# Kernel optimization log

Measured on AMD Instinct MI355X. Metric: run time of the kernel, lower is better.

Reference implementation:

```python
import jax, jax.numpy as jnp
import numpy as np

N_NODES = 100000
N_EDGES = 1600000
N_GRAPHS = 1024
D = 128
L = 3
BN_EPS = 1e-5


def setup_inputs() -> dict:
    key = jax.random.key(0)
    ks = jax.random.split(key, 16)
    x = jax.random.normal(ks[0], (N_NODES, D), dtype=jnp.float32)
    edge_index = jax.random.randint(ks[1], (2, N_EDGES), 0, N_NODES, dtype=jnp.int64)
    batch = jnp.sort(jax.random.randint(ks[2], (N_NODES,), 0, N_GRAPHS, dtype=jnp.int64))
    w = lambda k, shape: jax.random.normal(k, shape, dtype=jnp.float32) * 0.05
    return {
        "x": x,
        "edge_index": edge_index,
        "batch": batch,
        "conv_W1": w(ks[3], (L, D, D)),
        "conv_b1": w(ks[4], (L, D)),
        "bn_gamma": jax.random.uniform(ks[5], (L, D), dtype=jnp.float32) + 0.5,
        "bn_beta": w(ks[6], (L, D)),
        "bn_mean": w(ks[7], (L, D)),
        "bn_var": jax.random.uniform(ks[8], (L, D), dtype=jnp.float32) + 0.5,
        "conv_W2": w(ks[9], (L, D, D)),
        "conv_b2": w(ks[10], (L, D)),
        "head_W1": w(ks[11], (D, D)),
        "head_b1": w(ks[12], (D,)),
        "head_W2": w(ks[13], (D, D)),
        "head_b2": w(ks[14], (D,)),
    }


def reference(x, edge_index, batch, conv_W1, conv_b1, bn_gamma, bn_beta,
              bn_mean, bn_var, conv_W2, conv_b2, head_W1, head_b1,
              head_W2, head_b2):
    n = x.shape[0]
    src, dst = edge_index[0], edge_index[1]
    for l in range(L):
        # GINConv, eps=0: nn(x + sum_{j->i} x_j)
        agg = jax.ops.segment_sum(x[src], dst, num_segments=n)  # [N, D]
        h = x + agg
        # MLP([in, h, h]): Linear -> BatchNorm(eval) -> ReLU -> Linear
        h = h @ conv_W1[l] + conv_b1[l]
        h = (h - bn_mean[l]) * jax.lax.rsqrt(bn_var[l] + BN_EPS) * bn_gamma[l] + bn_beta[l]
        h = jax.nn.relu(h)
        h = h @ conv_W2[l] + conv_b2[l]
        x = jax.nn.relu(h)  # .relu() in the outer forward
    # global_add_pool over graph ids
    g = jax.ops.segment_sum(x, batch, num_segments=N_GRAPHS)  # [B, D]
    # head MLP (norm=None, dropout inactive at eval): Linear -> ReLU -> Linear
    g = jax.nn.relu(g @ head_W1 + head_b1)
    return g @ head_W2 + head_b2
```

## Files before the change

### kernel.cpp

```cpp
#include <hip/hip_runtime.h>

#define N_NODES  100000
#define N_EDGES  1600000
#define N_GRAPHS 1024
#define D        128
#define BN_EPS   1e-5f

#define FNSLICE      98
#define FSLICE_NODES 1024
#define FSLICE_CAP   20480
#define QCAP         96
#define CCHUNK       4000
#define CGRID        400

#define CVT_BLOCKS   6250
#define PW_BLOCKS    384
#define FOLD_BLOCKS  3
#define GST_BLOCKS   5
#define SETUP_GRID   (CVT_BLOCKS + PW_BLOCKS + FOLD_BLOCKS + GST_BLOCKS + 1)

typedef short bf16x8 __attribute__((ext_vector_type(8)));
typedef float f32x4  __attribute__((ext_vector_type(4)));

__device__ __forceinline__ ushort f2bf(float f) {
    unsigned int b = __float_as_uint(f);
    return (ushort)((b + 0x7fffu + ((b >> 16) & 1u)) >> 16);
}
__device__ __forceinline__ float bflo(unsigned int u) { return __uint_as_float(u << 16); }
__device__ __forceinline__ float bfhi(unsigned int u) { return __uint_as_float(u & 0xffff0000u); }
__device__ __forceinline__ unsigned int packbf(float x, float y) {
    return (unsigned int)f2bf(x) | ((unsigned int)f2bf(y) << 16);
}

__global__ __launch_bounds__(256) void setup_kernel(
        const float* __restrict__ x, ushort* __restrict__ xb,
        const float* __restrict__ W1, const float* __restrict__ W2,
        ushort* __restrict__ Wt,
        const float* __restrict__ b1, const float* __restrict__ gamma,
        const float* __restrict__ beta, const float* __restrict__ mean,
        const float* __restrict__ var, const float* __restrict__ b2,
        float* __restrict__ folds,
        const int* __restrict__ batch, int* __restrict__ gstart,
        int* __restrict__ slice_tail, int* __restrict__ offsets) {
    int b = blockIdx.x, t = threadIdx.x;
    if (b < CVT_BLOCKS) {
        size_t i = ((size_t)b * 256 + t) * 8;
        float4 v0 = *(const float4*)(x + i);
        float4 v1 = *(const float4*)(x + i + 4);
        uint4 o;
        o.x = packbf(v0.x, v0.y); o.y = packbf(v0.z, v0.w);
        o.z = packbf(v1.x, v1.y); o.w = packbf(v1.z, v1.w);
        *(uint4*)(xb + i) = o;
    } else if (b < CVT_BLOCKS + PW_BLOCKS) {
        int idx = (b - CVT_BLOCKS) * 256 + t;
        int i = idx >> 14, r = idx & 16383;
        int n = r >> 7, k = r & 127, l = i >> 1;
        const float* W = (i & 1) ? (W2 + (size_t)l * D * D) : (W1 + (size_t)l * D * D);
        Wt[idx] = f2bf(W[k * D + n]);
    } else if (b < CVT_BLOCKS + PW_BLOCKS + FOLD_BLOCKS) {
        int idx = (b - CVT_BLOCKS - PW_BLOCKS) * 256 + t;
        if (idx < 6 * D) {
            int i = idx >> 7, j = idx & 127, l = i >> 1;
            float s, o;
            if ((i & 1) == 0) {
                float sv = gamma[l * D + j] * rsqrtf(var[l * D + j] + BN_EPS);
                s = sv;
                o = (b1[l * D + j] - mean[l * D + j]) * sv + beta[l * D + j];
            } else {
                s = 1.0f;
                o = b2[l * D + j];
            }
            folds[(size_t)i * 2 * D + j]     = s;
            folds[(size_t)i * 2 * D + D + j] = o;
        }
    } else if (b < CVT_BLOCKS + PW_BLOCKS + FOLD_BLOCKS + GST_BLOCKS) {
        int g = (b - CVT_BLOCKS - PW_BLOCKS - FOLD_BLOCKS) * 256 + t;
        if (g <= N_GRAPHS) {
            int lo = 0, hi = N_NODES;
            while (lo < hi) {
                int mid = (lo + hi) >> 1;
                if (batch[mid] < g) lo = mid + 1; else hi = mid;
            }
            gstart[g] = lo;
        }
    } else {
        if (t < FNSLICE) slice_tail[t] = 0;
        if (t == 255) offsets[N_NODES] = N_EDGES;
    }
}

__global__ __launch_bounds__(256) void compact_kernel(const int* __restrict__ src,
                                                      const int* __restrict__ dst,
                                                      unsigned int* __restrict__ squeue,
                                                      int* __restrict__ slice_tail) {
    __shared__ unsigned int qbuf[FNSLICE * QCAP];
    __shared__ int qcnt[FNSLICE];
    __shared__ int qbase[FNSLICE];
    int t = threadIdx.x;
    for (int i = t; i < FNSLICE; i += 256) qcnt[i] = 0;
    __syncthreads();
    int e0 = blockIdx.x * CCHUNK;
    int eend = e0 + CCHUNK; if (eend > N_EDGES) eend = N_EDGES;
    for (int e = e0 + t; e < eend; e += 256) {
        int d = dst[e], s = src[e];
        int sl = d >> 10;
        unsigned int pk = ((unsigned int)(d & 1023) << 17) | (unsigned int)s;
        int pos = atomicAdd(&qcnt[sl], 1);
        if (pos < QCAP) qbuf[sl * QCAP + pos] = pk;
        else {
            int gp = atomicAdd(&slice_tail[sl], 1);
            squeue[(size_t)sl * FSLICE_CAP + gp] = pk;
        }
    }
    __syncthreads();
    for (int i = t; i < FNSLICE; i += 256) {
        int n = qcnt[i]; if (n > QCAP) n = QCAP;
        qbase[i] = atomicAdd(&slice_tail[i], n);
    }
    __syncthreads();
    int wv = t >> 6, ln = t & 63;
    for (int sl = wv; sl < FNSLICE; sl += 4) {
        int n = qcnt[sl]; if (n > QCAP) n = QCAP;
        int gb = qbase[sl];
        for (int i = ln; i < n; i += 64)
            squeue[(size_t)sl * FSLICE_CAP + gb + i] = qbuf[sl * QCAP + i];
    }
}

__global__ __launch_bounds__(1024) void fill_local(const unsigned int* __restrict__ squeue,
                                                   const int* __restrict__ slice_tail,
                                                   int* __restrict__ offsets,
                                                   int* __restrict__ csr_src) {
    __shared__ int hist[FSLICE_NODES];
    __shared__ int cur[FSLICE_NODES];
    __shared__ int sbase[128];
    __shared__ int wsum[16];
    int sl = blockIdx.x, t = threadIdx.x;
    int n = slice_tail[sl];
    if (t < 128) sbase[t] = (t < FNSLICE) ? slice_tail[t] : 0;
    hist[t] = 0;
    __syncthreads();
    for (int off = 1; off < 128; off <<= 1) {
        int u = (t < 128 && t >= off) ? sbase[t - off] : 0;
        __syncthreads();
        if (t < 128) sbase[t] += u;
        __syncthreads();
    }
    int gbase = (sl == 0) ? 0 : sbase[sl - 1];
    size_t qb = (size_t)sl * FSLICE_CAP;
    for (int i = t; i < n; i += 1024)
        atomicAdd(&hist[squeue[qb + i] >> 17], 1);
    __syncthreads();
    int c = hist[t];
    int lane = t & 63, w = t >> 6;
    int sc = c;
#pragma unroll
    for (int off = 1; off < 64; off <<= 1) {
        int u = __shfl_up(sc, off, 64);
        if (lane >= off) sc += u;
    }
    if (lane == 63) wsum[w] = sc;
    __syncthreads();
    if (t < 16) {
        int ws = wsum[t];
        int s2 = ws;
#pragma unroll
        for (int off = 1; off < 16; off <<= 1) {
            int u = __shfl_up(s2, off, 16);
            if (t >= off) s2 += u;
        }
        wsum[t] = s2 - ws;
    }
    __syncthreads();
    int gslot = gbase + sc + wsum[w] - c;
    cur[t] = gslot;
    int node = sl * FSLICE_NODES + t;
    if (node < N_NODES) offsets[node] = gslot;
    __syncthreads();
    for (int i = t; i < n; i += 1024) {
        unsigned int p = squeue[qb + i];
        int slot = atomicAdd(&cur[p >> 17], 1);
        csr_src[slot] = (int)(p & 0x1FFFFu);
    }
}

__global__ __launch_bounds__(256) void gather_bf16(const ushort* __restrict__ xb,
                                                   const int* __restrict__ offsets,
                                                   const int* __restrict__ csr_src,
                                                   ushort* __restrict__ hb) {
    int wv = threadIdx.x >> 6, lane = threadIdx.x & 63;
    int node = blockIdx.x * 4 + wv;
    const unsigned int* base = (const unsigned int*)xb;
    unsigned int u = base[(size_t)node * 64 + lane];
    float ax = bflo(u), ay = bfhi(u);
    int b = offsets[node], e = offsets[node + 1];
    int i = b;
    for (; i + 15 < e; i += 16) {
        int s0 = csr_src[i],      s1 = csr_src[i + 1],  s2 = csr_src[i + 2],  s3 = csr_src[i + 3];
        int s4 = csr_src[i + 4],  s5 = csr_src[i + 5],  s6 = csr_src[i + 6],  s7 = csr_src[i + 7];
        int s8 = csr_src[i + 8],  s9 = csr_src[i + 9],  sa = csr_src[i + 10], sb = csr_src[i + 11];
        int sc = csr_src[i + 12], sd = csr_src[i + 13], se = csr_src[i + 14], sf = csr_src[i + 15];
        unsigned int v0 = base[(size_t)s0 * 64 + lane];
        unsigned int v1 = base[(size_t)s1 * 64 + lane];
        unsigned int v2 = base[(size_t)s2 * 64 + lane];
        unsigned int v3 = base[(size_t)s3 * 64 + lane];
        unsigned int v4 = base[(size_t)s4 * 64 + lane];
        unsigned int v5 = base[(size_t)s5 * 64 + lane];
        unsigned int v6 = base[(size_t)s6 * 64 + lane];
        unsigned int v7 = base[(size_t)s7 * 64 + lane];
        unsigned int v8 = base[(size_t)s8 * 64 + lane];
        unsigned int v9 = base[(size_t)s9 * 64 + lane];
        unsigned int va = base[(size_t)sa * 64 + lane];
        unsigned int vb = base[(size_t)sb * 64 + lane];
        unsigned int vc = base[(size_t)sc * 64 + lane];
        unsigned int vd = base[(size_t)sd * 64 + lane];
        unsigned int ve = base[(size_t)se * 64 + lane];
        unsigned int vf = base[(size_t)sf * 64 + lane];
        ax += bflo(v0) + bflo(v1) + bflo(v2) + bflo(v3)
            + bflo(v4) + bflo(v5) + bflo(v6) + bflo(v7)
            + bflo(v8) + bflo(v9) + bflo(va) + bflo(vb)
            + bflo(vc) + bflo(vd) + bflo(ve) + bflo(vf);
        ay += bfhi(v0) + bfhi(v1) + bfhi(v2) + bfhi(v3)
            + bfhi(v4) + bfhi(v5) + bfhi(v6) + bfhi(v7)
            + bfhi(v8) + bfhi(v9) + bfhi(va) + bfhi(vb)
            + bfhi(vc) + bfhi(vd) + bfhi(ve) + bfhi(vf);
    }
    for (; i + 3 < e; i += 4) {
        int s0 = csr_src[i], s1 = csr_src[i + 1], s2 = csr_src[i + 2], s3 = csr_src[i + 3];
        unsigned int v0 = base[(size_t)s0 * 64 + lane];
        unsigned int v1 = base[(size_t)s1 * 64 + lane];
        unsigned int v2 = base[(size_t)s2 * 64 + lane];
        unsigned int v3 = base[(size_t)s3 * 64 + lane];
        ax += bflo(v0) + bflo(v1) + bflo(v2) + bflo(v3);
        ay += bfhi(v0) + bfhi(v1) + bfhi(v2) + bfhi(v3);
    }
    for (; i < e; ++i) {
        unsigned int v = base[(size_t)csr_src[i] * 64 + lane];
        ax += bflo(v); ay += bfhi(v);
    }
    ((unsigned int*)hb)[(size_t)node * 64 + lane] = packbf(ax, ay);
}

__global__ __launch_bounds__(512, 4) void fused_gemm(const ushort* __restrict__ in,
                                                     ushort* __restrict__ out,
                                                     const ushort* __restrict__ Wt1,
                                                     const ushort* __restrict__ Wt2,
                                                     const float* __restrict__ fold1,
                                                     const float* __restrict__ fold2) {
    __shared__ ushort As[128 * 136];
    __shared__ ushort Bs[128 * 136];
    int t = threadIdx.x;
    int row0 = blockIdx.x * 128;

#pragma unroll
    for (int i = 0; i < 4; ++i) {
        int f = t + 512 * i; int m = f >> 4, g = f & 15;
        *(float4*)(As + m * 136 + g * 8) = *(const float4*)(in + (size_t)(row0 + m) * D + g * 8);
        *(float4*)(Bs + m * 136 + g * 8) = *(const float4*)(Wt1 + (size_t)m * D + g * 8);
    }
    const uint4* w2v = (const uint4*)Wt2;
    uint4 p0 = w2v[t];
    uint4 p1 = w2v[t + 512];
    uint4 p2 = w2v[t + 1024];
    uint4 p3 = w2v[t + 1536];
    __syncthreads();

    int lane = t & 63, wv = t >> 6;
    int quad = lane >> 4, mr = lane & 15;
    int mbase = wv * 16;
    const ushort* ap = As + (mbase + mr) * 136 + quad * 8;
    bf16x8 a0 = *(const bf16x8*)(ap);
    bf16x8 a1 = *(const bf16x8*)(ap + 32);
    bf16x8 a2 = *(const bf16x8*)(ap + 64);
    bf16x8 a3 = *(const bf16x8*)(ap + 96);

#pragma unroll
    for (int nt = 0; nt < 8; ++nt) {
        const ushort* bq = Bs + (nt * 16 + mr) * 136 + quad * 8;
        bf16x8 b0 = *(const bf16x8*)(bq);
        bf16x8 b1 = *(const bf16x8*)(bq + 32);
        bf16x8 b2 = *(const bf16x8*)(bq + 64);
        bf16x8 b3 = *(const bf16x8*)(bq + 96);
        f32x4 acc = {0.f, 0.f, 0.f, 0.f};
        acc = __builtin_amdgcn_mfma_f32_16x16x32_bf16(a0, b0, acc, 0, 0, 0);
        acc = __builtin_amdgcn_mfma_f32_16x16x32_bf16(a1, b1, acc, 0, 0, 0);
        acc = __builtin_amdgcn_mfma_f32_16x16x32_bf16(a2, b2, acc, 0, 0, 0);
        acc = __builtin_amdgcn_mfma_f32_16x16x32_bf16(a3, b3, acc, 0, 0, 0);
        int j = nt * 16 + mr;
        float s = fold1[j], o = fold1[D + j];
#pragma unroll
        for (int r = 0; r < 4; ++r) {
            float z = fmaxf(fmaf(acc[r], s, o), 0.0f);
            As[(mbase + quad * 4 + r) * 136 + j] = f2bf(z);
        }
    }
    __syncthreads();

    {
        int f0 = t;          *(uint4*)(Bs + (f0 >> 4) * 136 + (f0 & 15) * 8) = p0;
        int f1 = t + 512;    *(uint4*)(Bs + (f1 >> 4) * 136 + (f1 & 15) * 8) = p1;
        int f2 = t + 1024;   *(uint4*)(Bs + (f2 >> 4) * 136 + (f2 & 15) * 8) = p2;
        int f3 = t + 1536;   *(uint4*)(Bs + (f3 >> 4) * 136 + (f3 & 15) * 8) = p3;
    }
    const ushort* hp = As + (mbase + mr) * 136 + quad * 8;
    bf16x8 h0 = *(const bf16x8*)(hp);
    bf16x8 h1 = *(const bf16x8*)(hp + 32);
    bf16x8 h2 = *(const bf16x8*)(hp + 64);
    bf16x8 h3 = *(const bf16x8*)(hp + 96);
    __syncthreads();

#pragma unroll
    for (int nt = 0; nt < 8; ++nt) {
        const ushort* bq = Bs + (nt * 16 + mr) * 136 + quad * 8;
        bf16x8 b0 = *(const bf16x8*)(bq);
        bf16x8 b1 = *(const bf16x8*)(bq + 32);
        bf16x8 b2 = *(const bf16x8*)(bq + 64);
        bf16x8 b3 = *(const bf16x8*)(bq + 96);
        f32x4 acc = {0.f, 0.f, 0.f, 0.f};
        acc = __builtin_amdgcn_mfma_f32_16x16x32_bf16(h0, b0, acc, 0, 0, 0);
        acc = __builtin_amdgcn_mfma_f32_16x16x32_bf16(h1, b1, acc, 0, 0, 0);
        acc = __builtin_amdgcn_mfma_f32_16x16x32_bf16(h2, b2, acc, 0, 0, 0);
        acc = __builtin_amdgcn_mfma_f32_16x16x32_bf16(h3, b3, acc, 0, 0, 0);
        int j = nt * 16 + mr;
        float o = fold2[D + j];
#pragma unroll
        for (int r = 0; r < 4; ++r) {
            float z = fmaxf(acc[r] + o, 0.0f);
            As[(mbase + quad * 4 + r) * 136 + j] = f2bf(z);
        }
    }
    __syncthreads();

#pragma unroll
    for (int i = 0; i < 8; ++i) {
        int f = t + 512 * i; int lr = f >> 5, g = f & 31;
        if (row0 + lr < N_NODES)
            *(float2*)(out + (size_t)(row0 + lr) * D + g * 4) =
                *(const float2*)(As + lr * 136 + g * 4);
    }
}

__global__ __launch_bounds__(128) void poolhead_kernel(const ushort* __restrict__ xb,
                                                       const int* __restrict__ gstart,
                                                       const float* __restrict__ W1,
                                                       const float* __restrict__ b1,
                                                       const float* __restrict__ W2,
                                                       const float* __restrict__ b2,
                                                       float* __restrict__ out) {
    __shared__ float row[128];
    __shared__ float t1[128];
    int r = blockIdx.x, j = threadIdx.x;
    float acc = 0.0f;
    int b = gstart[r], e = gstart[r + 1];
    for (int i = b; i < e; ++i)
        acc += __uint_as_float(((unsigned int)xb[(size_t)i * D + j]) << 16);
    row[j] = acc;
    __syncthreads();
    float a1 = b1[j];
    for (int k = 0; k < D; ++k) a1 = fmaf(row[k], W1[k * D + j], a1);
    t1[j] = fmaxf(a1, 0.0f);
    __syncthreads();
    float a2 = b2[j];
    for (int k = 0; k < D; ++k) a2 = fmaf(t1[k], W2[k * D + j], a2);
    out[r * D + j] = a2;
}

extern "C" void kernel_launch(void* const* d_in, const int* in_sizes, int n_in,
                              void* d_out, int out_size, void* d_ws, size_t ws_size,
                              hipStream_t stream) {
    const float* x        = (const float*)d_in[0];
    const int*   ei       = (const int*)d_in[1];
    const int*   src      = ei;
    const int*   dst      = ei + N_EDGES;
    const int*   batch    = (const int*)d_in[2];
    const float* conv_W1  = (const float*)d_in[3];
    const float* conv_b1  = (const float*)d_in[4];
    const float* bn_gamma = (const float*)d_in[5];
    const float* bn_beta  = (const float*)d_in[6];
    const float* bn_mean  = (const float*)d_in[7];
    const float* bn_var   = (const float*)d_in[8];
    const float* conv_W2  = (const float*)d_in[9];
    const float* conv_b2  = (const float*)d_in[10];
    const float* head_W1  = (const float*)d_in[11];
    const float* head_b1  = (const float*)d_in[12];
    const float* head_W2  = (const float*)d_in[13];
    const float* head_b2  = (const float*)d_in[14];
    float* out = (float*)d_out;

    char* ws = (char*)d_ws;
    size_t off = 0;
    auto alloc = [&](size_t bytes) -> void* {
        void* p = ws + off;
        off = (off + bytes + 255) & ~(size_t)255;
        return p;
    };
    const size_t NODE_BUF = (size_t)(N_NODES + 128) * D * sizeof(ushort);
    ushort* buf0    = (ushort*)alloc(NODE_BUF);
    ushort* buf1    = (ushort*)alloc(NODE_BUF);
    ushort* Wt      = (ushort*)alloc((size_t)6 * D * D * sizeof(ushort));
    float*  folds   = (float*)alloc((size_t)6 * 2 * D * sizeof(float));
    unsigned int* squeue = (unsigned int*)alloc((size_t)FNSLICE * FSLICE_CAP * sizeof(unsigned int));
    int*   csr_src  = (int*)alloc((size_t)(N_EDGES + 64) * sizeof(int));
    int*   offsets  = (int*)alloc((size_t)(N_NODES + 1) * sizeof(int));
    int*   slice_tail = (int*)alloc((size_t)FNSLICE * sizeof(int));
    int*   gstart   = (int*)alloc((size_t)(N_GRAPHS + 1) * sizeof(int));

    setup_kernel<<<SETUP_GRID, 256, 0, stream>>>(
        x, buf0, conv_W1, conv_W2, Wt,
        conv_b1, bn_gamma, bn_beta, bn_mean, bn_var, conv_b2, folds,
        batch, gstart, slice_tail, offsets);
    compact_kernel<<<CGRID, 256, 0, stream>>>(src, dst, squeue, slice_tail);
    fill_local<<<FNSLICE, 1024, 0, stream>>>(squeue, slice_tail, offsets, csr_src);

    const int FUSED_GRID = (N_NODES + 127) / 128;
    for (int l = 0; l < 3; ++l) {
        gather_bf16<<<N_NODES / 4, 256, 0, stream>>>(buf0, offsets, csr_src, buf1);
        fused_gemm<<<FUSED_GRID, 512, 0, stream>>>(buf1, buf0,
            Wt + (size_t)(2 * l) * D * D, Wt + (size_t)(2 * l + 1) * D * D,
            folds + (size_t)(2 * l) * 2 * D, folds + (size_t)(2 * l + 1) * 2 * D);
    }

    poolhead_kernel<<<N_GRAPHS, 128, 0, stream>>>(buf0, gstart, head_W1, head_b1,
                                                  head_W2, head_b2, out);
}
```

Baseline: 445.5 us.

## Fuse neighbor gather into GEMM kernel, writing aggregates directly to LDS

Merges the separate gather kernel into the fused MLP kernel. Each wave aggregates its 16 rows of neighbor features straight into the shared-memory A tile, so the intermediate aggregate buffer is never written to or read back from global memory and one launch per layer disappears. Output buffers now ping-pong. The trade-off is that each block's MFMA stage waits on irregular gathers, and with 512-thread blocks and heavy LDS use there may be less latency hiding than the former 25000 small gather blocks had.

```diff
diff --git a/kernel.cpp b/kernel.cpp
--- a/kernel.cpp
+++ b/kernel.cpp
@@ -184,80 +184,85 @@
     }
 }
 
-__global__ __launch_bounds__(256) void gather_bf16(const ushort* __restrict__ xb,
-                                                   const int* __restrict__ offsets,
-                                                   const int* __restrict__ csr_src,
-                                                   ushort* __restrict__ hb) {
-    int wv = threadIdx.x >> 6, lane = threadIdx.x & 63;
-    int node = blockIdx.x * 4 + wv;
-    const unsigned int* base = (const unsigned int*)xb;
-    unsigned int u = base[(size_t)node * 64 + lane];
-    float ax = bflo(u), ay = bfhi(u);
-    int b = offsets[node], e = offsets[node + 1];
-    int i = b;
-    for (; i + 15 < e; i += 16) {
-        int s0 = csr_src[i],      s1 = csr_src[i + 1],  s2 = csr_src[i + 2],  s3 = csr_src[i + 3];
-        int s4 = csr_src[i + 4],  s5 = csr_src[i + 5],  s6 = csr_src[i + 6],  s7 = csr_src[i + 7];
-        int s8 = csr_src[i + 8],  s9 = csr_src[i + 9],  sa = csr_src[i + 10], sb = csr_src[i + 11];
-        int sc = csr_src[i + 12], sd = csr_src[i + 13], se = csr_src[i + 14], sf = csr_src[i + 15];
-        unsigned int v0 = base[(size_t)s0 * 64 + lane];
-        unsigned int v1 = base[(size_t)s1 * 64 + lane];
-        unsigned int v2 = base[(size_t)s2 * 64 + lane];
-        unsigned int v3 = base[(size_t)s3 * 64 + lane];
-        unsigned int v4 = base[(size_t)s4 * 64 + lane];
-        unsigned int v5 = base[(size_t)s5 * 64 + lane];
-        unsigned int v6 = base[(size_t)s6 * 64 + lane];
-        unsigned int v7 = base[(size_t)s7 * 64 + lane];
-        unsigned int v8 = base[(size_t)s8 * 64 + lane];
-        unsigned int v9 = base[(size_t)s9 * 64 + lane];
-        unsigned int va = base[(size_t)sa * 64 + lane];
-        unsigned int vb = base[(size_t)sb * 64 + lane];
-        unsigned int vc = base[(size_t)sc * 64 + lane];
-        unsigned int vd = base[(size_t)sd * 64 + lane];
-        unsigned int ve = base[(size_t)se * 64 + lane];
-        unsigned int vf = base[(size_t)sf * 64 + lane];
-        ax += bflo(v0) + bflo(v1) + bflo(v2) + bflo(v3)
-            + bflo(v4) + bflo(v5) + bflo(v6) + bflo(v7)
-            + bflo(v8) + bflo(v9) + bflo(va) + bflo(vb)
-            + bflo(vc) + bflo(vd) + bflo(ve) + bflo(vf);
-        ay += bfhi(v0) + bfhi(v1) + bfhi(v2) + bfhi(v3)
-            + bfhi(v4) + bfhi(v5) + bfhi(v6) + bfhi(v7)
-            + bfhi(v8) + bfhi(v9) + bfhi(va) + bfhi(vb)
-            + bfhi(vc) + bfhi(vd) + bfhi(ve) + bfhi(vf);
-    }
-    for (; i + 3 < e; i += 4) {
-        int s0 = csr_src[i], s1 = csr_src[i + 1], s2 = csr_src[i + 2], s3 = csr_src[i + 3];
-        unsigned int v0 = base[(size_t)s0 * 64 + lane];
-        unsigned int v1 = base[(size_t)s1 * 64 + lane];
-        unsigned int v2 = base[(size_t)s2 * 64 + lane];
-        unsigned int v3 = base[(size_t)s3 * 64 + lane];
-        ax += bflo(v0) + bflo(v1) + bflo(v2) + bflo(v3);
-        ay += bfhi(v0) + bfhi(v1) + bfhi(v2) + bfhi(v3);
-    }
-    for (; i < e; ++i) {
-        unsigned int v = base[(size_t)csr_src[i] * 64 + lane];
-        ax += bflo(v); ay += bfhi(v);
-    }
-    ((unsigned int*)hb)[(size_t)node * 64 + lane] = packbf(ax, ay);
-}
-
-__global__ __launch_bounds__(512, 4) void fused_gemm(const ushort* __restrict__ in,
-                                                     ushort* __restrict__ out,
-                                                     const ushort* __restrict__ Wt1,
-                                                     const ushort* __restrict__ Wt2,
-                                                     const float* __restrict__ fold1,
-                                                     const float* __restrict__ fold2) {
+__global__ __launch_bounds__(512, 4) void gin_layer(const ushort* __restrict__ in,
+                                                    ushort* __restrict__ out,
+                                                    const int* __restrict__ offsets,
+                                                    const int* __restrict__ csr_src,
+                                                    const ushort* __restrict__ Wt1,
+                                                    const ushort* __restrict__ Wt2,
+                                                    const float* __restrict__ fold1,
+                                                    const float* __restrict__ fold2) {
     __shared__ ushort As[128 * 136];
     __shared__ ushort Bs[128 * 136];
     int t = threadIdx.x;
     int row0 = blockIdx.x * 128;
+    int lane = t & 63, wv = t >> 6;
+    int mbase = wv * 16;
 
 #pragma unroll
     for (int i = 0; i < 4; ++i) {
         int f = t + 512 * i; int m = f >> 4, g = f & 15;
-        *(float4*)(As + m * 136 + g * 8) = *(const float4*)(in + (size_t)(row0 + m) * D + g * 8);
         *(float4*)(Bs + m * 136 + g * 8) = *(const float4*)(Wt1 + (size_t)m * D + g * 8);
     }
+
+    const unsigned int* base = (const unsigned int*)in;
+    unsigned int* asu = (unsigned int*)As;
+#pragma unroll 1
+    for (int rr = 0; rr < 16; ++rr) {
+        int node = row0 + mbase + rr;
+        float ax = 0.0f, ay = 0.0f;
+        if (node < N_NODES) {
+            unsigned int u = base[(size_t)node * 64 + lane];
+            ax = bflo(u); ay = bfhi(u);
+            int bo = offsets[node], e = offsets[node + 1];
+            int i = bo;
+            for (; i + 15 < e; i += 16) {
+                int s0 = csr_src[i],      s1 = csr_src[i + 1],  s2 = csr_src[i + 2],  s3 = csr_src[i + 3];
+                int s4 = csr_src[i + 4],  s5 = csr_src[i + 5],  s6 = csr_src[i + 6],  s7 = csr_src[i + 7];
+                int s8 = csr_src[i + 8],  s9 = csr_src[i + 9],  sa = csr_src[i + 10], sb = csr_src[i + 11];
+                int sc = csr_src[i + 12], sd = csr_src[i + 13], se = csr_src[i + 14], sf = csr_src[i + 15];
+                unsigned int v0 = base[(size_t)s0 * 64 + lane];
+                unsigned int v1 = base[(size_t)s1 * 64 + lane];
+                unsigned int v2 = base[(size_t)s2 * 64 + lane];
+                unsigned int v3 = base[(size_t)s3 * 64 + lane];
+                unsigned int v4 = base[(size_t)s4 * 64 + lane];
+                unsigned int v5 = base[(size_t)s5 * 64 + lane];
+                unsigned int v6 = base[(size_t)s6 * 64 + lane];
+                unsigned int v7 = base[(size_t)s7 * 64 + lane];
+                unsigned int v8 = base[(size_t)s8 * 64 + lane];
+                unsigned int v9 = base[(size_t)s9 * 64 + lane];
+                unsigned int va = base[(size_t)sa * 64 + lane];
+                unsigned int vb = base[(size_t)sb * 64 + lane];
+                unsigned int vc = base[(size_t)sc * 64 + lane];
+                unsigned int vd = base[(size_t)sd * 64 + lane];
+                unsigned int ve = base[(size_t)se * 64 + lane];
+                unsigned int vf = base[(size_t)sf * 64 + lane];
+                ax += bflo(v0) + bflo(v1) + bflo(v2) + bflo(v3)
+                    + bflo(v4) + bflo(v5) + bflo(v6) + bflo(v7)
+                    + bflo(v8) + bflo(v9) + bflo(va) + bflo(vb)
+                    + bflo(vc) + bflo(vd) + bflo(ve) + bflo(vf);
+                ay += bfhi(v0) + bfhi(v1) + bfhi(v2) + bfhi(v3)
+                    + bfhi(v4) + bfhi(v5) + bfhi(v6) + bfhi(v7)
+                    + bfhi(v8) + bfhi(v9) + bfhi(va) + bfhi(vb)
+                    + bfhi(vc) + bfhi(vd) + bfhi(ve) + bfhi(vf);
+            }
+            for (; i + 3 < e; i += 4) {
+                int s0 = csr_src[i], s1 = csr_src[i + 1], s2 = csr_src[i + 2], s3 = csr_src[i + 3];
+                unsigned int v0 = base[(size_t)s0 * 64 + lane];
+                unsigned int v1 = base[(size_t)s1 * 64 + lane];
+                unsigned int v2 = base[(size_t)s2 * 64 + lane];
+                unsigned int v3 = base[(size_t)s3 * 64 + lane];
+                ax += bflo(v0) + bflo(v1) + bflo(v2) + bflo(v3);
+                ay += bfhi(v0) + bfhi(v1) + bfhi(v2) + bfhi(v3);
+            }
+            for (; i < e; ++i) {
+                unsigned int v = base[(size_t)csr_src[i] * 64 + lane];
+                ax += bflo(v); ay += bfhi(v);
+            }
+        }
+        asu[(mbase + rr) * 68 + lane] = packbf(ax, ay);
+    }
+
     const uint4* w2v = (const uint4*)Wt2;
     uint4 p0 = w2v[t];
     uint4 p1 = w2v[t + 512];
@@ -265,9 +270,7 @@
     uint4 p3 = w2v[t + 1536];
     __syncthreads();
 
-    int lane = t & 63, wv = t >> 6;
     int quad = lane >> 4, mr = lane & 15;
-    int mbase = wv * 16;
     const ushort* ap = As + (mbase + mr) * 136 + quad * 8;
     bf16x8 a0 = *(const bf16x8*)(ap);
     bf16x8 a1 = *(const bf16x8*)(ap + 32);
@@ -413,13 +416,15 @@
     fill_local<<<FNSLICE, 1024, 0, stream>>>(squeue, slice_tail, offsets, csr_src);
 
     const int FUSED_GRID = (N_NODES + 127) / 128;
+    ushort* cur = buf0;
+    ushort* nxt = buf1;
     for (int l = 0; l < 3; ++l) {
-        gather_bf16<<<N_NODES / 4, 256, 0, stream>>>(buf0, offsets, csr_src, buf1);
-        fused_gemm<<<FUSED_GRID, 512, 0, stream>>>(buf1, buf0,
+        gin_layer<<<FUSED_GRID, 512, 0, stream>>>(cur, nxt, offsets, csr_src,
             Wt + (size_t)(2 * l) * D * D, Wt + (size_t)(2 * l + 1) * D * D,
             folds + (size_t)(2 * l) * 2 * D, folds + (size_t)(2 * l + 1) * 2 * D);
-    }
-
-    poolhead_kernel<<<N_GRAPHS, 128, 0, stream>>>(buf0, gstart, head_W1, head_b1,
+        ushort* tmp = cur; cur = nxt; nxt = tmp;
+    }
+
+    poolhead_kernel<<<N_GRAPHS, 128, 0, stream>>>(cur, gstart, head_W1, head_b1,
                                                   head_W2, head_b2, out);
 }
```

Measured after the change: 541.5 us. +21.5%, slower.

## Fold edge compaction into setup kernel and gather two nodes per wavefront

Applied to the files above, without the earlier changes.

The edge-compaction kernel now runs as extra blocks inside the setup launch, and slice_tail is zeroed by a memset issued beforehand. This removes one kernel launch and lets compaction overlap with conversion work. The gather kernel now has each wavefront handle two consecutive nodes, interleaving their neighbour loads 8 at a time so more independent memory requests are in flight. The cost is a smaller grid with more registers per thread, and every setup block now reserves compaction shared memory, which may reduce occupancy for the conversion blocks.

```diff
diff --git a/kernel.cpp b/kernel.cpp
--- a/kernel.cpp
+++ b/kernel.cpp
@@ -17,7 +17,11 @@
 #define PW_BLOCKS    384
 #define FOLD_BLOCKS  3
 #define GST_BLOCKS   5
-#define SETUP_GRID   (CVT_BLOCKS + PW_BLOCKS + FOLD_BLOCKS + GST_BLOCKS + 1)
+#define MISC_BASE    (CVT_BLOCKS + PW_BLOCKS + FOLD_BLOCKS + GST_BLOCKS)
+#define COMPACT_BASE (MISC_BASE + 1)
+#define SETUP_GRID   (COMPACT_BASE + CGRID)
+
+#define GATHER_GRID  12500
 
 typedef short bf16x8 __attribute__((ext_vector_type(8)));
 typedef float f32x4  __attribute__((ext_vector_type(4)));
@@ -41,7 +45,12 @@
         const float* __restrict__ var, const float* __restrict__ b2,
         float* __restrict__ folds,
         const int* __restrict__ batch, int* __restrict__ gstart,
-        int* __restrict__ slice_tail, int* __restrict__ offsets) {
+        int* __restrict__ slice_tail, int* __restrict__ offsets,
+        const int* __restrict__ src, const int* __restrict__ dst,
+        unsigned int* __restrict__ squeue) {
+    __shared__ unsigned int qbuf[FNSLICE * QCAP];
+    __shared__ int qcnt[FNSLICE];
+    __shared__ int qbase[FNSLICE];
     int b = blockIdx.x, t = threadIdx.x;
     if (b < CVT_BLOCKS) {
         size_t i = ((size_t)b * 256 + t) * 8;
@@ -73,7 +82,7 @@
             folds[(size_t)i * 2 * D + j]     = s;
             folds[(size_t)i * 2 * D + D + j] = o;
         }
-    } else if (b < CVT_BLOCKS + PW_BLOCKS + FOLD_BLOCKS + GST_BLOCKS) {
+    } else if (b < MISC_BASE) {
         int g = (b - CVT_BLOCKS - PW_BLOCKS - FOLD_BLOCKS) * 256 + t;
         if (g <= N_GRAPHS) {
             int lo = 0, hi = N_NODES;
@@ -83,47 +92,37 @@
             }
             gstart[g] = lo;
         }
+    } else if (b == MISC_BASE) {
+        if (t == 255) offsets[N_NODES] = N_EDGES;
     } else {
-        if (t < FNSLICE) slice_tail[t] = 0;
-        if (t == 255) offsets[N_NODES] = N_EDGES;
-    }
-}
-
-__global__ __launch_bounds__(256) void compact_kernel(const int* __restrict__ src,
-                                                      const int* __restrict__ dst,
-                                                      unsigned int* __restrict__ squeue,
-                                                      int* __restrict__ slice_tail) {
-    __shared__ unsigned int qbuf[FNSLICE * QCAP];
-    __shared__ int qcnt[FNSLICE];
-    __shared__ int qbase[FNSLICE];
-    int t = threadIdx.x;
-    for (int i = t; i < FNSLICE; i += 256) qcnt[i] = 0;
-    __syncthreads();
-    int e0 = blockIdx.x * CCHUNK;
-    int eend = e0 + CCHUNK; if (eend > N_EDGES) eend = N_EDGES;
-    for (int e = e0 + t; e < eend; e += 256) {
-        int d = dst[e], s = src[e];
-        int sl = d >> 10;
-        unsigned int pk = ((unsigned int)(d & 1023) << 17) | (unsigned int)s;
-        int pos = atomicAdd(&qcnt[sl], 1);
-        if (pos < QCAP) qbuf[sl * QCAP + pos] = pk;
-        else {
-            int gp = atomicAdd(&slice_tail[sl], 1);
-            squeue[(size_t)sl * FSLICE_CAP + gp] = pk;
-        }
-    }
-    __syncthreads();
-    for (int i = t; i < FNSLICE; i += 256) {
-        int n = qcnt[i]; if (n > QCAP) n = QCAP;
-        qbase[i] = atomicAdd(&slice_tail[i], n);
-    }
-    __syncthreads();
-    int wv = t >> 6, ln = t & 63;
-    for (int sl = wv; sl < FNSLICE; sl += 4) {
-        int n = qcnt[sl]; if (n > QCAP) n = QCAP;
-        int gb = qbase[sl];
-        for (int i = ln; i < n; i += 64)
-            squeue[(size_t)sl * FSLICE_CAP + gb + i] = qbuf[sl * QCAP + i];
+        for (int i = t; i < FNSLICE; i += 256) qcnt[i] = 0;
+        __syncthreads();
+        int e0 = (b - COMPACT_BASE) * CCHUNK;
+        int eend = e0 + CCHUNK; if (eend > N_EDGES) eend = N_EDGES;
+        for (int e = e0 + t; e < eend; e += 256) {
+            int d = dst[e], s = src[e];
+            int sl = d >> 10;
+            unsigned int pk = ((unsigned int)(d & 1023) << 17) | (unsigned int)s;
+            int pos = atomicAdd(&qcnt[sl], 1);
+            if (pos < QCAP) qbuf[sl * QCAP + pos] = pk;
+            else {
+                int gp = atomicAdd(&slice_tail[sl], 1);
+                squeue[(size_t)sl * FSLICE_CAP + gp] = pk;
+            }
+        }
+        __syncthreads();
+        for (int i = t; i < FNSLICE; i += 256) {
+            int n = qcnt[i]; if (n > QCAP) n = QCAP;
+            qbase[i] = atomicAdd(&slice_tail[i], n);
+        }
+        __syncthreads();
+        int wv = t >> 6, ln = t & 63;
+        for (int sl = wv; sl < FNSLICE; sl += 4) {
+            int n = qcnt[sl]; if (n > QCAP) n = QCAP;
+            int gb = qbase[sl];
+            for (int i = ln; i < n; i += 64)
+                squeue[(size_t)sl * FSLICE_CAP + gb + i] = qbuf[sl * QCAP + i];
+        }
     }
 }
 
@@ -184,22 +183,15 @@
     }
 }
 
-__global__ __launch_bounds__(256) void gather_bf16(const ushort* __restrict__ xb,
-                                                   const int* __restrict__ offsets,
-                                                   const int* __restrict__ csr_src,
-                                                   ushort* __restrict__ hb) {
-    int wv = threadIdx.x >> 6, lane = threadIdx.x & 63;
-    int node = blockIdx.x * 4 + wv;
-    const unsigned int* base = (const unsigned int*)xb;
-    unsigned int u = base[(size_t)node * 64 + lane];
-    float ax = bflo(u), ay = bfhi(u);
-    int b = offsets[node], e = offsets[node + 1];
-    int i = b;
+__device__ __forceinline__ void drain_stream(const unsigned int* __restrict__ base,
+                                             const int* __restrict__ csr,
+                                             int i, int e, int lane,
+                                             float& ax, float& ay) {
     for (; i + 15 < e; i += 16) {
-        int s0 = csr_src[i],      s1 = csr_src[i + 1],  s2 = csr_src[i + 2],  s3 = csr_src[i + 3];
-        int s4 = csr_src[i + 4],  s5 = csr_src[i + 5],  s6 = csr_src[i + 6],  s7 = csr_src[i + 7];
-        int s8 = csr_src[i + 8],  s9 = csr_src[i + 9],  sa = csr_src[i + 10], sb = csr_src[i + 11];
-        int sc = csr_src[i + 12], sd = csr_src[i + 13], se = csr_src[i + 14], sf = csr_src[i + 15];
+        int s0 = csr[i],      s1 = csr[i + 1],  s2 = csr[i + 2],  s3 = csr[i + 3];
+        int s4 = csr[i + 4],  s5 = csr[i + 5],  s6 = csr[i + 6],  s7 = csr[i + 7];
+        int s8 = csr[i + 8],  s9 = csr[i + 9],  sa = csr[i + 10], sb = csr[i + 11];
+        int sc = csr[i + 12], sd = csr[i + 13], se = csr[i + 14], sf = csr[i + 15];
         unsigned int v0 = base[(size_t)s0 * 64 + lane];
         unsigned int v1 = base[(size_t)s1 * 64 + lane];
         unsigned int v2 = base[(size_t)s2 * 64 + lane];
@@ -226,7 +218,7 @@
             + bfhi(vc) + bfhi(vd) + bfhi(ve) + bfhi(vf);
     }
     for (; i + 3 < e; i += 4) {
-        int s0 = csr_src[i], s1 = csr_src[i + 1], s2 = csr_src[i + 2], s3 = csr_src[i + 3];
+        int s0 = csr[i], s1 = csr[i + 1], s2 = csr[i + 2], s3 = csr[i + 3];
         unsigned int v0 = base[(size_t)s0 * 64 + lane];
         unsigned int v1 = base[(size_t)s1 * 64 + lane];
         unsigned int v2 = base[(size_t)s2 * 64 + lane];
@@ -235,10 +227,65 @@
         ay += bfhi(v0) + bfhi(v1) + bfhi(v2) + bfhi(v3);
     }
     for (; i < e; ++i) {
-        unsigned int v = base[(size_t)csr_src[i] * 64 + lane];
+        unsigned int v = base[(size_t)csr[i] * 64 + lane];
         ax += bflo(v); ay += bfhi(v);
     }
-    ((unsigned int*)hb)[(size_t)node * 64 + lane] = packbf(ax, ay);
+}
+
+__global__ __launch_bounds__(256) void gather_bf16(const ushort* __restrict__ xb,
+                                                   const int* __restrict__ offsets,
+                                                   const int* __restrict__ csr_src,
+                                                   ushort* __restrict__ hb) {
+    int wv = threadIdx.x >> 6, lane = threadIdx.x & 63;
+    int n0 = (blockIdx.x * 4 + wv) * 2;
+    const unsigned int* base = (const unsigned int*)xb;
+    unsigned int u0 = base[(size_t)n0 * 64 + lane];
+    unsigned int u1 = base[(size_t)(n0 + 1) * 64 + lane];
+    float ax0 = bflo(u0), ay0 = bfhi(u0);
+    float ax1 = bflo(u1), ay1 = bfhi(u1);
+    int i0 = offsets[n0];
+    int e0 = offsets[n0 + 1];
+    int i1 = e0;
+    int e1 = offsets[n0 + 2];
+    while (i0 + 7 < e0 && i1 + 7 < e1) {
+        int s0 = csr_src[i0],     s1 = csr_src[i0 + 1],
+            s2 = csr_src[i0 + 2], s3 = csr_src[i0 + 3];
+        int s4 = csr_src[i0 + 4], s5 = csr_src[i0 + 5],
+            s6 = csr_src[i0 + 6], s7 = csr_src[i0 + 7];
+        int r0 = csr_src[i1],     r1 = csr_src[i1 + 1],
+            r2 = csr_src[i1 + 2], r3 = csr_src[i1 + 3];
+        int r4 = csr_src[i1 + 4], r5 = csr_src[i1 + 5],
+            r6 = csr_src[i1 + 6], r7 = csr_src[i1 + 7];
+        unsigned int v0 = base[(size_t)s0 * 64 + lane];
+        unsigned int v1 = base[(size_t)s1 * 64 + lane];
+        unsigned int v2 = base[(size_t)s2 * 64 + lane];
+        unsigned int v3 = base[(size_t)s3 * 64 + lane];
+        unsigned int v4 = base[(size_t)s4 * 64 + lane];
+        unsigned int v5 = base[(size_t)s5 * 64 + lane];
+        unsigned int v6 = base[(size_t)s6 * 64 + lane];
+        unsigned int v7 = base[(size_t)s7 * 64 + lane];
+        unsigned int w0 = base[(size_t)r0 * 64 + lane];
+        unsigned int w1 = base[(size_t)r1 * 64 + lane];
+        unsigned int w2 = base[(size_t)r2 * 64 + lane];
+        unsigned int w3 = base[(size_t)r3 * 64 + lane];
+        unsigned int w4 = base[(size_t)r4 * 64 + lane];
+        unsigned int w5 = base[(size_t)r5 * 64 + lane];
+        unsigned int w6 = base[(size_t)r6 * 64 + lane];
+        unsigned int w7 = base[(size_t)r7 * 64 + lane];
+        ax0 += bflo(v0) + bflo(v1) + bflo(v2) + bflo(v3)
+             + bflo(v4) + bflo(v5) + bflo(v6) + bflo(v7);
+        ay0 += bfhi(v0) + bfhi(v1) + bfhi(v2) + bfhi(v3)
+             + bfhi(v4) + bfhi(v5) + bfhi(v6) + bfhi(v7);
+        ax1 += bflo(w0) + bflo(w1) + bflo(w2) + bflo(w3)
+             + bflo(w4) + bflo(w5) + bflo(w6) + bflo(w7);
+        ay1 += bfhi(w0) + bfhi(w1) + bfhi(w2) + bfhi(w3)
+             + bfhi(w4) + bfhi(w5) + bfhi(w6) + bfhi(w7);
+        i0 += 8; i1 += 8;
+    }
+    drain_stream(base, csr_src, i0, e0, lane, ax0, ay0);
+    drain_stream(base, csr_src, i1, e1, lane, ax1, ay1);
+    ((unsigned int*)hb)[(size_t)n0 * 64 + lane]       = packbf(ax0, ay0);
+    ((unsigned int*)hb)[(size_t)(n0 + 1) * 64 + lane] = packbf(ax1, ay1);
 }
 
 __global__ __launch_bounds__(512, 4) void fused_gemm(const ushort* __restrict__ in,
@@ -405,16 +452,16 @@
     int*   slice_tail = (int*)alloc((size_t)FNSLICE * sizeof(int));
     int*   gstart   = (int*)alloc((size_t)(N_GRAPHS + 1) * sizeof(int));
 
+    hipMemsetAsync(slice_tail, 0, FNSLICE * sizeof(int), stream);
     setup_kernel<<<SETUP_GRID, 256, 0, stream>>>(
         x, buf0, conv_W1, conv_W2, Wt,
         conv_b1, bn_gamma, bn_beta, bn_mean, bn_var, conv_b2, folds,
-        batch, gstart, slice_tail, offsets);
-    compact_kernel<<<CGRID, 256, 0, stream>>>(src, dst, squeue, slice_tail);
+        batch, gstart, slice_tail, offsets, src, dst, squeue);
     fill_local<<<FNSLICE, 1024, 0, stream>>>(squeue, slice_tail, offsets, csr_src);
 
     const int FUSED_GRID = (N_NODES + 127) / 128;
     for (int l = 0; l < 3; ++l) {
-        gather_bf16<<<N_NODES / 4, 256, 0, stream>>>(buf0, offsets, csr_src, buf1);
+        gather_bf16<<<GATHER_GRID, 256, 0, stream>>>(buf0, offsets, csr_src, buf1);
         fused_gemm<<<FUSED_GRID, 512, 0, stream>>>(buf1, buf0,
             Wt + (size_t)(2 * l) * D * D, Wt + (size_t)(2 * l + 1) * D * D,
             folds + (size_t)(2 * l) * 2 * D, folds + (size_t)(2 * l + 1) * 2 * D);
```

Result: no change. 439.6 us (-1.3%).
